# Kernel tuning notes

Hardware: AMD Instinct MI355X
Metric: run time of the kernel (lower is better)

## Reference

```python
import jax, jax.numpy as jnp
import numpy as np

FP8_MAX = 448.0  # torch.finfo(torch.float8_e4m3fn).max
FP8_MIN = -448.0
EPS = 1e-12


def fp8_quantize(x):
    """Scalar (per-tensor) dynamic fp8 e4m3 quantization, matching fp8_quantize(scalar=True).
    Returns fp8-rounded values (stored as float32) and the reciprocal scale (float32)."""
    amax = jnp.clip(jnp.max(jnp.abs(x)), EPS, None)
    scale = FP8_MAX / amax
    q = jnp.clip(x * scale, FP8_MIN, FP8_MAX)
    q = q.astype(jnp.float8_e4m3fn).astype(jnp.float32)  # rounding to fp8 grid
    return q, (1.0 / scale).astype(jnp.float32)


def setup_inputs() -> dict:
    key = jax.random.key(0)
    k_in, k_w, k_b = jax.random.split(key, 3)
    M, K, N = 16384, 2048, 2048
    input = jax.random.normal(k_in, (M, K), dtype=jnp.float32)
    weight = jax.random.normal(k_w, (N, K), dtype=jnp.float32) * 0.02
    # from_unquant: quantize weight once at init
    qweight, w_scale = fp8_quantize(weight)
    bias = jax.random.normal(k_b, (N,), dtype=jnp.float32) * 0.01
    return {"input": input, "qweight": qweight, "w_scale": w_scale, "bias": bias}


def reference(input, qweight, w_scale, bias):
    # dynamic per-tensor fp8 quantization of the activation
    qinput, a_scale = fp8_quantize(input)  # [M, K], scalar
    # torch._scaled_mm(qinput, qweight.t(), scale_a, scale_b, bias):
    #   out = (A_fp8 @ B_fp8) * scale_a * scale_b + bias, in out_dtype
    out = jnp.matmul(qinput, qweight.T)  # [M, N]
    out = out * (a_scale * w_scale) + bias[None, :]
    return out.astype(jnp.float32)
```

## Files before the change

kernel.cpp:

```cpp
#include <hip/hip_runtime.h>

typedef float f32x4 __attribute__((ext_vector_type(4)));
typedef int   i32x4 __attribute__((ext_vector_type(4)));
typedef int   i32x8 __attribute__((ext_vector_type(8)));

#define FP8MAX 448.0f
#define AMAX_BLOCKS 2048
#define WQ_BLOCKS 512


__device__ __forceinline__ unsigned pack_fp8_exact(float4 v) {
    int r = __builtin_amdgcn_cvt_pk_fp8_f32(v.x, v.y, 0, false);
    return (unsigned)__builtin_amdgcn_cvt_pk_fp8_f32(v.z, v.w, r, true);
}

__global__ __launch_bounds__(256) void amax_and_wquant(
    const float4* __restrict__ x, float* __restrict__ partial, int n4,
    const float4* __restrict__ w, uint4* __restrict__ qw, int n16w) {
    if (blockIdx.x < AMAX_BLOCKS) {
        float m0 = 0.0f, m1 = 0.0f;
        int stride = AMAX_BLOCKS * 256;
        int i = blockIdx.x * 256 + threadIdx.x;
        for (; i + stride < n4; i += 2 * stride) {
            float4 a = x[i];
            float4 b = x[i + stride];
            m0 = fmaxf(m0, fmaxf(fmaxf(fabsf(a.x), fabsf(a.y)), fmaxf(fabsf(a.z), fabsf(a.w))));
            m1 = fmaxf(m1, fmaxf(fmaxf(fabsf(b.x), fabsf(b.y)), fmaxf(fabsf(b.z), fabsf(b.w))));
        }
        if (i < n4) {
            float4 a = x[i];
            m0 = fmaxf(m0, fmaxf(fmaxf(fabsf(a.x), fabsf(a.y)), fmaxf(fabsf(a.z), fabsf(a.w))));
        }
        float m = fmaxf(m0, m1);
#pragma unroll
        for (int off = 32; off > 0; off >>= 1)
            m = fmaxf(m, __shfl_down(m, off, 64));
        __shared__ float ws[4];
        if ((threadIdx.x & 63) == 0) ws[threadIdx.x >> 6] = m;
        __syncthreads();
        if (threadIdx.x == 0)
            partial[blockIdx.x] = fmaxf(fmaxf(ws[0], ws[1]), fmaxf(ws[2], ws[3]));
    } else {
        int stride = WQ_BLOCKS * 256;
        for (int i = (blockIdx.x - AMAX_BLOCKS) * 256 + threadIdx.x; i < n16w; i += stride) {
            uint4 r;
            r.x = pack_fp8_exact(w[i * 4 + 0]);
            r.y = pack_fp8_exact(w[i * 4 + 1]);
            r.z = pack_fp8_exact(w[i * 4 + 2]);
            r.w = pack_fp8_exact(w[i * 4 + 3]);
            qw[i] = r;
        }
    }
}


__device__ __forceinline__ float reduce_partials(const float* __restrict__ partial) {
    float m = 0.0f;
#pragma unroll
    for (int j = 0; j < AMAX_BLOCKS / 256; ++j)
        m = fmaxf(m, partial[threadIdx.x + j * 256]);
#pragma unroll
    for (int off = 32; off > 0; off >>= 1)
        m = fmaxf(m, __shfl_down(m, off, 64));
    __shared__ float ws[4];
    if ((threadIdx.x & 63) == 0) ws[threadIdx.x >> 6] = m;
    __syncthreads();
    return fmaxf(fmaxf(ws[0], ws[1]), fmaxf(ws[2], ws[3]));
}

__device__ __forceinline__ unsigned pack_fp8_clip(float4 v, float s) {
    float a = fminf(fmaxf(v.x * s, -FP8MAX), FP8MAX);
    float b = fminf(fmaxf(v.y * s, -FP8MAX), FP8MAX);
    float c = fminf(fmaxf(v.z * s, -FP8MAX), FP8MAX);
    float d = fminf(fmaxf(v.w * s, -FP8MAX), FP8MAX);
    int r = __builtin_amdgcn_cvt_pk_fp8_f32(a, b, 0, false);
    r = __builtin_amdgcn_cvt_pk_fp8_f32(c, d, r, true);
    return (unsigned)r;
}

__global__ __launch_bounds__(256) void quant_act(
    const float4* __restrict__ x, uint4* __restrict__ q,
    const float* __restrict__ partial, unsigned* __restrict__ amax_bits, int n16) {
    float amax = fmaxf(reduce_partials(partial), 1e-12f);
    if (blockIdx.x == 0 && threadIdx.x == 0)
        *amax_bits = __float_as_uint(amax);
    float s = FP8MAX / amax;
    int i = blockIdx.x * blockDim.x + threadIdx.x;
    if (i >= n16) return;
    uint4 r;
    r.x = pack_fp8_clip(x[i * 4 + 0], s);
    r.y = pack_fp8_clip(x[i * 4 + 1], s);
    r.z = pack_fp8_clip(x[i * 4 + 2], s);
    r.w = pack_fp8_clip(x[i * 4 + 3], s);
    q[i] = r;
}


__global__ __launch_bounds__(256) void gemm_fp8_mx(
    const unsigned char* __restrict__ Aq,
    const unsigned char* __restrict__ Bq,
    const unsigned* __restrict__ amax_bits,
    const float* __restrict__ w_scale_p,
    const float* __restrict__ bias,
    float* __restrict__ C,
    int M, int N, int K) {
    __shared__ unsigned char lA[128 * 128];
    __shared__ unsigned char lB[128 * 128];

    const int tid = threadIdx.x;
    const int lane = tid & 63;
    const int wave = tid >> 6;

    const int bn = blockIdx.x;
    const int bm = blockIdx.y;
    const int row0 = bm * 128;
    const int col0 = bn * 128;

    const int wm = wave >> 1;
    const int wn = wave & 1;
    const int m_base = wm * 64;
    const int n_base = wn * 64;

    const int lane_lo = lane & 15;
    const int h = lane >> 4;
    const int c0 = 2 * h;
    const int c1 = 2 * h + 1;

    f32x4 acc[4][4];
#pragma unroll
    for (int i = 0; i < 4; ++i)
#pragma unroll
        for (int j = 0; j < 4; ++j)
            acc[i][j] = (f32x4){0.f, 0.f, 0.f, 0.f};

    union frag8 { i32x8 v; i32x4 half[2]; };

    for (int k0 = 0; k0 < K; k0 += 128) {
#pragma unroll
        for (int it = 0; it < 4; ++it) {
            int chunk = tid + it * 256;
            int r = chunk >> 3;
            int cpos = chunk & 7;
            int csrc = cpos ^ (r & 7);
            const unsigned char* gA = Aq + (size_t)(row0 + r) * K + (k0 + csrc * 16);
            const unsigned char* gB = Bq + (size_t)(col0 + r) * K + (k0 + csrc * 16);
            __builtin_amdgcn_global_load_lds(
                (const __attribute__((address_space(1))) void*)gA,
                (__attribute__((address_space(3))) void*)(lA + chunk * 16), 16, 0, 0);
            __builtin_amdgcn_global_load_lds(
                (const __attribute__((address_space(1))) void*)gB,
                (__attribute__((address_space(3))) void*)(lB + chunk * 16), 16, 0, 0);
        }
        __syncthreads();

        frag8 af[4], bf[4];
#pragma unroll
        for (int i = 0; i < 4; ++i) {
            int m = m_base + i * 16 + lane_lo;
            int p0 = c0 ^ (m & 7);
            int p1 = c1 ^ (m & 7);
            af[i].half[0] = *(const i32x4*)(lA + m * 128 + p0 * 16);
            af[i].half[1] = *(const i32x4*)(lA + m * 128 + p1 * 16);
        }
#pragma unroll
        for (int j = 0; j < 4; ++j) {
            int n = n_base + j * 16 + lane_lo;
            int p0 = c0 ^ (n & 7);
            int p1 = c1 ^ (n & 7);
            bf[j].half[0] = *(const i32x4*)(lB + n * 128 + p0 * 16);
            bf[j].half[1] = *(const i32x4*)(lB + n * 128 + p1 * 16);
        }
#pragma unroll
        for (int i = 0; i < 4; ++i)
#pragma unroll
            for (int j = 0; j < 4; ++j)
                acc[i][j] = __builtin_amdgcn_mfma_scale_f32_16x16x128_f8f6f4(
                    af[i].v, bf[j].v, acc[i][j],
                    0, 0,
                    0, 0x7F7F7F7F,
                    0, 0x7F7F7F7F);
        __syncthreads();
    }

    float amax = fmaxf(__uint_as_float(*amax_bits), 1e-12f);
    float scale = FP8MAX / amax;
    float a_scale = 1.0f / scale;
    float s = a_scale * w_scale_p[0];

    const int lane_hi = lane >> 4;
#pragma unroll
    for (int i = 0; i < 4; ++i) {
#pragma unroll
        for (int j = 0; j < 4; ++j) {
            int col = col0 + n_base + j * 16 + lane_lo;
            float bv = bias[col];
#pragma unroll
            for (int r = 0; r < 4; ++r) {
                int row = row0 + m_base + i * 16 + lane_hi * 4 + r;
                C[(size_t)row * N + col] = acc[i][j][r] * s + bv;
            }
        }
    }
}


extern "C" void kernel_launch(void* const* d_in, const int* in_sizes, int n_in,
                              void* d_out, int out_size, void* d_ws, size_t ws_size,
                              hipStream_t stream) {
    const float* input   = (const float*)d_in[0];
    const float* qweight = (const float*)d_in[1];
    const float* w_scale = (const float*)d_in[2];
    const float* bias    = (const float*)d_in[3];
    float* out = (float*)d_out;

    const int N = in_sizes[3];
    const int K = in_sizes[1] / N;
    const int M = in_sizes[0] / K;

    unsigned* amax_bits = (unsigned*)d_ws;
    float* partial = (float*)((char*)d_ws + 256);
    unsigned char* qA = (unsigned char*)d_ws + 16384;
    unsigned char* qW = qA + (size_t)M * K;

    const int n4a  = (M / 4) * K;
    const int n16w = (N / 4) * K / 4;
    hipLaunchKernelGGL(amax_and_wquant, dim3(AMAX_BLOCKS + WQ_BLOCKS), dim3(256), 0, stream,
                       (const float4*)input, partial, n4a,
                       (const float4*)qweight, (uint4*)qW, n16w);

    const int n16a = n4a / 4;
    hipLaunchKernelGGL(quant_act, dim3((n16a + 255) / 256), dim3(256), 0, stream,
                       (const float4*)input, (uint4*)qA, partial, amax_bits, n16a);

    hipLaunchKernelGGL(gemm_fp8_mx, dim3(N / 128, M / 128), dim3(256), 0, stream,
                       qA, qW, amax_bits, w_scale, bias, out, M, N, K);
}
```

Measured before the change: 325.8 us.

## Fuse activation fp8 quantization into GEMM tile loading

```diff
diff --git a/kernel.cpp b/kernel.cpp
--- a/kernel.cpp
+++ b/kernel.cpp
@@ -78,28 +78,11 @@
     return (unsigned)r;
 }
 
-__global__ __launch_bounds__(256) void quant_act(
-    const float4* __restrict__ x, uint4* __restrict__ q,
-    const float* __restrict__ partial, unsigned* __restrict__ amax_bits, int n16) {
-    float amax = fmaxf(reduce_partials(partial), 1e-12f);
-    if (blockIdx.x == 0 && threadIdx.x == 0)
-        *amax_bits = __float_as_uint(amax);
-    float s = FP8MAX / amax;
-    int i = blockIdx.x * blockDim.x + threadIdx.x;
-    if (i >= n16) return;
-    uint4 r;
-    r.x = pack_fp8_clip(x[i * 4 + 0], s);
-    r.y = pack_fp8_clip(x[i * 4 + 1], s);
-    r.z = pack_fp8_clip(x[i * 4 + 2], s);
-    r.w = pack_fp8_clip(x[i * 4 + 3], s);
-    q[i] = r;
-}
-
-
-__global__ __launch_bounds__(256) void gemm_fp8_mx(
-    const unsigned char* __restrict__ Aq,
+
+__global__ __launch_bounds__(256) void gemm_fp8_fusedq(
+    const float* __restrict__ X,
     const unsigned char* __restrict__ Bq,
-    const unsigned* __restrict__ amax_bits,
+    const float* __restrict__ partial,
     const float* __restrict__ w_scale_p,
     const float* __restrict__ bias,
     float* __restrict__ C,
@@ -107,6 +90,9 @@
     __shared__ unsigned char lA[128 * 128];
     __shared__ unsigned char lB[128 * 128];
 
+    float amax = fmaxf(reduce_partials(partial), 1e-12f);
+    float s_q = FP8MAX / amax;
+
     const int tid = threadIdx.x;
     const int lane = tid & 63;
     const int wave = tid >> 6;
@@ -142,14 +128,28 @@
             int r = chunk >> 3;
             int cpos = chunk & 7;
             int csrc = cpos ^ (r & 7);
-            const unsigned char* gA = Aq + (size_t)(row0 + r) * K + (k0 + csrc * 16);
             const unsigned char* gB = Bq + (size_t)(col0 + r) * K + (k0 + csrc * 16);
-            __builtin_amdgcn_global_load_lds(
-                (const __attribute__((address_space(1))) void*)gA,
-                (__attribute__((address_space(3))) void*)(lA + chunk * 16), 16, 0, 0);
             __builtin_amdgcn_global_load_lds(
                 (const __attribute__((address_space(1))) void*)gB,
                 (__attribute__((address_space(3))) void*)(lB + chunk * 16), 16, 0, 0);
+        }
+#pragma unroll
+        for (int it = 0; it < 4; ++it) {
+            int chunk = tid + it * 256;
+            int r = chunk >> 3;
+            int cpos = chunk & 7;
+            int csrc = cpos ^ (r & 7);
+            const float4* gA = (const float4*)(X + (size_t)(row0 + r) * K + (k0 + csrc * 16));
+            float4 a0 = gA[0];
+            float4 a1 = gA[1];
+            float4 a2 = gA[2];
+            float4 a3 = gA[3];
+            uint4 qa;
+            qa.x = pack_fp8_clip(a0, s_q);
+            qa.y = pack_fp8_clip(a1, s_q);
+            qa.z = pack_fp8_clip(a2, s_q);
+            qa.w = pack_fp8_clip(a3, s_q);
+            *(uint4*)(lA + chunk * 16) = qa;
         }
         __syncthreads();
 
@@ -182,9 +182,7 @@
         __syncthreads();
     }
 
-    float amax = fmaxf(__uint_as_float(*amax_bits), 1e-12f);
-    float scale = FP8MAX / amax;
-    float a_scale = 1.0f / scale;
+    float a_scale = 1.0f / s_q;
     float s = a_scale * w_scale_p[0];
 
     const int lane_hi = lane >> 4;
@@ -217,10 +215,8 @@
     const int K = in_sizes[1] / N;
     const int M = in_sizes[0] / K;
 
-    unsigned* amax_bits = (unsigned*)d_ws;
     float* partial = (float*)((char*)d_ws + 256);
-    unsigned char* qA = (unsigned char*)d_ws + 16384;
-    unsigned char* qW = qA + (size_t)M * K;
+    unsigned char* qW = (unsigned char*)d_ws + 16384;
 
     const int n4a  = (M / 4) * K;
     const int n16w = (N / 4) * K / 4;
@@ -228,10 +224,6 @@
                        (const float4*)input, partial, n4a,
                        (const float4*)qweight, (uint4*)qW, n16w);
 
-    const int n16a = n4a / 4;
-    hipLaunchKernelGGL(quant_act, dim3((n16a + 255) / 256), dim3(256), 0, stream,
-                       (const float4*)input, (uint4*)qA, partial, amax_bits, n16a);
-
-    hipLaunchKernelGGL(gemm_fp8_mx, dim3(N / 128, M / 128), dim3(256), 0, stream,
-                       qA, qW, amax_bits, w_scale, bias, out, M, N, K);
-}
+    hipLaunchKernelGGL(gemm_fp8_fusedq, dim3(N / 128, M / 128), dim3(256), 0, stream,
+                       input, qW, partial, w_scale, bias, out, M, N, K);
+}
```

New measurement: 443.5 us. 36.2% more time.
